# Kernel tuning notes

Measured on AMD Instinct MI355X. Metric: run time of the kernel, lower is better.

The kernel has to match this reference:

```python
import jax, jax.numpy as jnp
import numpy as np

E = 1024   # embed_dim
H = 16     # num_heads
D = E // H # head_dim
B = 2
S = 2048
YAT_EPS = 0.1


def setup_inputs() -> dict:
    key = jax.random.key(0)
    ks = jax.random.split(key, 5)
    w_scale = (6.0 / (E + E)) ** 0.5  # xavier_uniform bound
    def xavier(k):
        return jax.random.uniform(k, (E, E), jnp.float32, -w_scale, w_scale)
    return {
        "x": jax.random.normal(ks[0], (B, S, E), jnp.float32),
        "Wq": xavier(ks[1]), "bq": jnp.zeros((E,), jnp.float32),
        "Wk": xavier(ks[2]), "bk": jnp.zeros((E,), jnp.float32),
        "Wv": xavier(ks[3]), "bv": jnp.zeros((E,), jnp.float32),
        "Wo": xavier(ks[4]), "bo": jnp.zeros((E,), jnp.float32),
    }


def reference(x, Wq, bq, Wk, bk, Wv, bv, Wo, bo):
    b, s, _ = x.shape
    # Projections (Linear: x @ W + b, flax kernel layout [in, out])
    Q = x @ Wq + bq
    K = x @ Wk + bk
    V = x @ Wv + bv
    # [B, H, S, D]
    Q = Q.reshape(b, s, H, D).transpose(0, 2, 1, 3)
    K = K.reshape(b, s, H, D).transpose(0, 2, 1, 3)
    V = V.reshape(b, s, H, D).transpose(0, 2, 1, 3)
    # L2 normalize along head_dim
    Qn = Q / (jnp.linalg.norm(Q, axis=-1, keepdims=True) + 1e-8)
    Kn = K / (jnp.linalg.norm(K, axis=-1, keepdims=True) + 1e-8)
    # Yat kernel scores: (1 + <q,k>)^2 / (eps + (1 - <q,k>))
    dot = jnp.einsum("bhqd,bhkd->bhqk", Qn, Kn)
    scores = (1.0 + dot) ** 2 / (YAT_EPS + (1.0 - dot))
    # Sum-normalize (no softmax)
    attn = scores / (jnp.sum(scores, axis=-1, keepdims=True) + 1e-6)
    out = jnp.einsum("bhqk,bhkd->bhqd", attn, V)
    out = out.transpose(0, 2, 1, 3).reshape(b, s, E)
    return out @ Wo + bo
```

## Files before the change

### kernel.cpp

```cpp
#include <hip/hip_runtime.h>
#include <math.h>

#define EDIM 1024
#define NH   16
#define HD   64
#define BATCH 2
#define SEQ  2048
#define NROW (BATCH*SEQ)
#define YAT_EPS 0.1f

typedef _Float16 f16;
typedef _Float16 f16x8 __attribute__((ext_vector_type(8)));
typedef _Float16 f16x4 __attribute__((ext_vector_type(4)));
typedef __fp16   h16x2 __attribute__((ext_vector_type(2)));
typedef float    f32x4 __attribute__((ext_vector_type(4)));

static __device__ __forceinline__ int pk2(float a, float b) {
    union { h16x2 h; int i; } u;
    u.h = __builtin_amdgcn_cvt_pkrtz(a, b);
    return u.i;
}

static __device__ __forceinline__ void gload16(const f16* g, f16* l) {
    __builtin_amdgcn_global_load_lds(
        (const __attribute__((address_space(1))) void*)g,
        (__attribute__((address_space(3))) void*)l,
        16, 0, 0);
}

__global__ __launch_bounds__(256)
void prep_kernel(const float* __restrict__ x, f16* __restrict__ xb,
                 const float* __restrict__ W0, const float* __restrict__ W1,
                 const float* __restrict__ W2, const float* __restrict__ W3,
                 f16* __restrict__ T0, f16* __restrict__ T1,
                 f16* __restrict__ T2, f16* __restrict__ T3)
{
    const int z = blockIdx.z;
    if (z == 4) {
        const int bid = blockIdx.y * 32 + blockIdx.x;
#pragma unroll
        for (int i = 0; i < 4; ++i) {
            const int off = bid * 4096 + i * 1024 + threadIdx.x * 4;
            const float4 v = *(const float4*)(x + off);
            union { int i2[2]; f16x4 h; } o;
            o.i2[0] = pk2(v.x, v.y);
            o.i2[1] = pk2(v.z, v.w);
            *(f16x4*)(xb + off) = o.h;
        }
        return;
    }
    const float* W = (z == 0) ? W0 : (z == 1) ? W1 : (z == 2) ? W2 : W3;
    f16*         Wt = (z == 0) ? T0 : (z == 1) ? T1 : (z == 2) ? T2 : T3;

    __shared__ float T[32][33];
    const int t = threadIdx.x;
    const int r = t >> 3, c4 = (t & 7) * 4;
    const int bi = blockIdx.x * 32, bj = blockIdx.y * 32;
    const float4 v = *(const float4*)(W + (size_t)(bi + r) * 1024 + bj + c4);
    T[r][c4 + 0] = v.x; T[r][c4 + 1] = v.y; T[r][c4 + 2] = v.z; T[r][c4 + 3] = v.w;
    __syncthreads();
    f16x4 o = {(f16)T[c4 + 0][r], (f16)T[c4 + 1][r], (f16)T[c4 + 2][r], (f16)T[c4 + 3][r]};
    *(f16x4*)(Wt + (size_t)(bj + r) * 1024 + bi + c4) = o;
}

template<int BM, int BN, int WM>
__global__ __launch_bounds__(WM * 128, 3)
void gemm_f16(const f16* __restrict__ A,
              const f16* __restrict__ B0, const f16* __restrict__ B1, const f16* __restrict__ B2,
              const float* __restrict__ bi0, const float* __restrict__ bi1, const float* __restrict__ bi2,
              void* __restrict__ o0, void* __restrict__ o1, void* __restrict__ o2,
              int e0, int e1, int e2)
{
    constexpr int NT    = WM * 128;
    constexpr int SR    = NT / 4;
    constexpr int ASL   = BM / SR;
    constexpr int BSL   = BN / SR;
    constexpr int ABUF  = BM * 32;
    constexpr int BBUF  = BN * 32;
    constexpr int WROWS = BM / WM;
    constexpr int MT    = WROWS / 16;
    constexpr int HALVES = BN / 128;
    constexpr int SCH    = 2048 / NT;
    __shared__ __align__(16) char lds[2 * (ABUF + BBUF) * 2];
    f16* As = (f16*)lds;
    f16* Bs = (f16*)lds + 2 * ABUF;

    const int z = blockIdx.z;
    const f16*   Bt   = (z == 0) ? B0  : (z == 1) ? B1  : B2;
    const float* bias = (z == 0) ? bi0 : (z == 1) ? bi1 : bi2;
    void*        Cout = (z == 0) ? o0  : (z == 1) ? o1  : o2;
    const int    epi  = (z == 0) ? e0  : (z == 1) ? e1  : e2;

    const int tid  = threadIdx.x;
    const int lane = tid & 63;
    const int w    = tid >> 6;
    const int cl   = lane & 15;
    const int quad = lane >> 4;
    const int wm = w % WM, wn = w / WM;
    const int bm = blockIdx.x * BM, bn = blockIdx.y * BN;
    const int wmoff = wm * WROWS;

    const int srow = tid >> 2;
    const int sc   = tid & 3;
    const int scg  = (sc ^ (srow & 3)) * 8;
    const f16* gA = A  + (size_t)(bm + srow) * 1024 + scg;
    const f16* gB = Bt + (size_t)(bn + srow) * 1024 + scg;
    f16* lA[ASL]; f16* lB[BSL];
#pragma unroll
    for (int i = 0; i < ASL; ++i) lA[i] = As + (srow + i * SR) * 32 + sc * 8;
#pragma unroll
    for (int i = 0; i < BSL; ++i) lB[i] = Bs + (srow + i * SR) * 32 + sc * 8;

    f32x4 acc[MT][4];
#pragma unroll
    for (int i = 0; i < MT; ++i)
#pragma unroll
        for (int j = 0; j < 4; ++j) acc[i][j] = (f32x4){0.f, 0.f, 0.f, 0.f};

#pragma unroll
    for (int i = 0; i < ASL; ++i) gload16(gA + (size_t)i * SR * 1024, lA[i]);
#pragma unroll
    for (int i = 0; i < BSL; ++i) gload16(gB + (size_t)i * SR * 1024, lB[i]);
    __syncthreads();

    const int fsw = (quad ^ (cl & 3)) * 8;

    for (int it = 0; it < 32; ++it) {
        const int buf = it & 1, nb = buf ^ 1;
        if (it < 31) {
            const int kn = (it + 1) * 32;
#pragma unroll
            for (int i = 0; i < ASL; ++i)
                gload16(gA + (size_t)i * SR * 1024 + kn, lA[i] + nb * ABUF);
#pragma unroll
            for (int i = 0; i < BSL; ++i)
                gload16(gB + (size_t)i * SR * 1024 + kn, lB[i] + nb * BBUF);
        }
        f16x8 af[MT], bf[4];
#pragma unroll
        for (int mt = 0; mt < MT; ++mt)
            af[mt] = *(const f16x8*)(&As[buf * ABUF + (wmoff + mt * 16 + cl) * 32 + fsw]);
#pragma unroll
        for (int nt = 0; nt < 4; ++nt)
            bf[nt] = *(const f16x8*)(&Bs[buf * BBUF + (wn * 64 + nt * 16 + cl) * 32 + fsw]);
#pragma unroll
        for (int mt = 0; mt < MT; ++mt)
#pragma unroll
            for (int nt = 0; nt < 4; ++nt)
                acc[mt][nt] = __builtin_amdgcn_mfma_f32_16x16x32_f16(af[mt], bf[nt], acc[mt][nt], 0, 0, 0);
        __syncthreads();
    }

    float bcol[4];
#pragma unroll
    for (int nt = 0; nt < 4; ++nt) bcol[nt] = bias[bn + wn * 64 + nt * 16 + cl];
#pragma unroll
    for (int mt = 0; mt < MT; ++mt)
#pragma unroll
        for (int nt = 0; nt < 4; ++nt)
#pragma unroll
            for (int rg = 0; rg < 4; ++rg) acc[mt][nt][rg] += bcol[nt];

    const int b_idx = bm >> 11, sl0 = bm & (SEQ - 1), h0 = bn >> 6;

    if (epi == 0) {
        float* C = (float*)Cout;
#pragma unroll
        for (int mt = 0; mt < MT; ++mt)
#pragma unroll
            for (int rg = 0; rg < 4; ++rg) {
                const int row = bm + wmoff + mt * 16 + quad * 4 + rg;
#pragma unroll
                for (int nt = 0; nt < 4; ++nt)
                    C[(size_t)row * EDIM + bn + wn * 64 + nt * 16 + cl] = acc[mt][nt][rg];
            }
    } else if (epi == 1) {
        if constexpr (BM == 128) {
        f16* C = (f16*)Cout;
        f16* S = (f16*)lds;
#pragma unroll
        for (int h = 0; h < HALVES; ++h) {
            __syncthreads();
            if ((wn >> 1) == h) {
#pragma unroll
                for (int mt = 0; mt < MT; ++mt)
#pragma unroll
                    for (int rg = 0; rg < 4; ++rg) {
                        float ss = 0.f;
#pragma unroll
                        for (int nt = 0; nt < 4; ++nt) ss += acc[mt][nt][rg] * acc[mt][nt][rg];
                        ss += __shfl_xor(ss, 1); ss += __shfl_xor(ss, 2);
                        ss += __shfl_xor(ss, 4); ss += __shfl_xor(ss, 8);
                        const float inv = 1.0f / (sqrtf(ss) + 1e-8f);
                        const int row = wmoff + mt * 16 + quad * 4 + rg;
#pragma unroll
                        for (int nt = 0; nt < 4; ++nt) {
                            const int colh = (wn & 1) * 64 + nt * 16 + cl;
                            S[row * 128 + (((colh >> 3) ^ (row & 15)) * 8) + (colh & 7)] =
                                (f16)(acc[mt][nt][rg] * inv);
                        }
                    }
            }
            __syncthreads();
#pragma unroll
            for (int i = 0; i < SCH; ++i) {
                const int c = tid + i * NT;
                const int s = c >> 4, gi = c & 15;
                f16x8 v = *(const f16x8*)(&S[s * 128 + ((gi ^ (s & 15)) * 8)]);
                const int head = h0 + h * 2 + (gi >> 3), d8 = (gi & 7) * 8;
                *(f16x8*)(C + ((size_t)(b_idx * NH + head) * SEQ + sl0 + s) * HD + d8) = v;
            }
        }
        }
    } else {
        if constexpr (BM == 128) {
        f16* C = (f16*)Cout;
        f16* S = (f16*)lds;
#pragma unroll
        for (int h = 0; h < HALVES; ++h) {
            __syncthreads();
            if ((wn >> 1) == h) {
#pragma unroll
                for (int mt = 0; mt < MT; ++mt) {
                    const int s0 = wmoff + mt * 16 + quad * 4;
#pragma unroll
                    for (int nt = 0; nt < 4; ++nt) {
                        const int colh = (wn & 1) * 64 + nt * 16 + cl;
                        f16x4 o = {(f16)acc[mt][nt][0], (f16)acc[mt][nt][1],
                                   (f16)acc[mt][nt][2], (f16)acc[mt][nt][3]};
                        *(f16x4*)(&S[colh * 128 + (((s0 >> 3) ^ (colh & 15)) * 8) + (s0 & 7)]) = o;
                    }
                }
            }
            __syncthreads();
#pragma unroll
            for (int i = 0; i < SCH; ++i) {
                const int c = tid + i * NT;
                const int colh = c >> 4, gi = c & 15;
                f16x8 v = *(const f16x8*)(&S[colh * 128 + ((gi ^ (colh & 15)) * 8)]);
                const int head = h0 + h * 2 + (colh >> 6), d = colh & 63;
                *(f16x8*)(C + ((size_t)(b_idx * NH + head) * HD + d) * SEQ + sl0 + gi * 8) = v;
            }
        }
        }
    }
}

__global__ __launch_bounds__(512, 4)
void yat_attn(const f16* __restrict__ Qh, const f16* __restrict__ Kh,
              const f16* __restrict__ Vt, f16* __restrict__ AO)
{
    __shared__ __align__(16) char lds[49152];
    f16* Qs = (f16*)lds;
    f16* KB = (f16*)(lds + 16384);
    f16* VB = (f16*)(lds + 32768);

    const int tid  = threadIdx.x;
    const int lane = tid & 63;
    const int w    = tid >> 6;
    const int cl   = lane & 15;
    const int quad = lane >> 4;
    const int wm = w & 3;
    const int wk = w >> 2;
    const int q0 = blockIdx.x * 128;
    const int bh = blockIdx.y;

    const f16* Qg = Qh + (size_t)bh * SEQ * HD;
    const f16* Kg = Kh + (size_t)bh * SEQ * HD;
    const f16* Vg = Vt + (size_t)bh * HD * SEQ;

    const int rkv = tid >> 3;
    const int gkv = tid & 7;
    const f16* gK = Kg + (size_t)rkv * HD + gkv * 8;
    const f16* gV = Vg + (size_t)rkv * SEQ + gkv * 8;
    const int lkOff = rkv * 64 + ((gkv ^ (rkv & 7)) * 8);

    f16x8 kr = *(const f16x8*)(gK);
    f16x8 vr = *(const f16x8*)(gV);

#pragma unroll
    for (int i = 0; i < 2; ++i) {
        const int s0 = tid + i * 512;
        const int row = s0 >> 3, g = s0 & 7;
        f16x8 v = *(const f16x8*)(Qg + (size_t)(q0 + row) * HD + g * 8);
        *(f16x8*)(&Qs[row * 64 + ((g ^ (row & 7)) * 8)]) = v;
    }
    __syncthreads();
    f16x8 qf[2][2];
#pragma unroll
    for (int qt = 0; qt < 2; ++qt)
#pragma unroll
        for (int kb = 0; kb < 2; ++kb)
            qf[qt][kb] = *(const f16x8*)(&Qs[(wm * 32 + qt * 16 + cl) * 64 +
                                             ((kb * 4 + quad) ^ (cl & 7)) * 8]);

    f32x4 O[2][4];
    float rs[2] = {0.f, 0.f};
#pragma unroll
    for (int i = 0; i < 2; ++i)
#pragma unroll
        for (int j = 0; j < 4; ++j) O[i][j] = (f32x4){0.f, 0.f, 0.f, 0.f};

    for (int t = 0; t < 32; ++t) {
        const int buf = t & 1;
        *(f16x8*)(&KB[buf * 4096 + lkOff]) = kr;
        *(f16x8*)(&VB[buf * 4096 + lkOff]) = vr;
        if (t < 31) {
            kr = *(const f16x8*)(gK + (size_t)(t + 1) * 64 * HD);
            vr = *(const f16x8*)(gV + (t + 1) * 64);
        }
        __syncthreads();

        const f16* Ks = KB + buf * 4096;
        const f16* Vs = VB + buf * 4096;

        f32x4 s[2][2];
#pragma unroll
        for (int kt = 0; kt < 2; ++kt)
#pragma unroll
            for (int qt = 0; qt < 2; ++qt) s[kt][qt] = (f32x4){0.f, 0.f, 0.f, 0.f};
#pragma unroll
        for (int kb = 0; kb < 2; ++kb) {
            const int sw = ((kb * 4 + quad) ^ (cl & 7)) * 8;
            f16x8 af0 = *(const f16x8*)(&Ks[(wk * 32 +  0 + cl) * 64 + sw]);
            f16x8 af1 = *(const f16x8*)(&Ks[(wk * 32 + 16 + cl) * 64 + sw]);
#pragma unroll
            for (int qt = 0; qt < 2; ++qt) {
                s[0][qt] = __builtin_amdgcn_mfma_f32_16x16x32_f16(af0, qf[qt][kb], s[0][qt], 0, 0, 0);
                s[1][qt] = __builtin_amdgcn_mfma_f32_16x16x32_f16(af1, qf[qt][kb], s[1][qt], 0, 0, 0);
            }
        }

        f16x4 pa16[2][2];
#pragma unroll
        for (int kt = 0; kt < 2; ++kt)
#pragma unroll
            for (int qt = 0; qt < 2; ++qt) {
                float p[4];
#pragma unroll
                for (int rg = 0; rg < 4; ++rg) {
                    const float u = (1.0f + YAT_EPS) - s[kt][qt][rg];
                    p[rg] = fmaf(4.41f, __builtin_amdgcn_rcpf(u), u - 4.2f);
                    rs[qt] += p[rg];
                }
                union { int i2[2]; f16x4 h; } pk_;
                pk_.i2[0] = pk2(p[0], p[1]);
                pk_.i2[1] = pk2(p[2], p[3]);
                pa16[kt][qt] = pk_.h;
            }

#pragma unroll
        for (int kt = 0; kt < 2; ++kt)
#pragma unroll
            for (int dn = 0; dn < 4; ++dn) {
                const int row = dn * 16 + cl;
                const int g = wk * 4 + kt * 2 + (quad >> 1);
                f16x4 vb = *(const f16x4*)(&Vs[row * 64 + ((g ^ (row & 7)) * 8) + (quad & 1) * 4]);
#pragma unroll
                for (int qt = 0; qt < 2; ++qt)
                    O[qt][dn] = __builtin_amdgcn_mfma_f32_16x16x16f16(pa16[kt][qt], vb, O[qt][dn], 0, 0, 0);
            }
    }

    __syncthreads();
    float* rs_s = (float*)lds;
    float* Ox   = (float*)(lds + 1024);

#pragma unroll
    for (int qt = 0; qt < 2; ++qt) {
        float t = rs[qt];
        t += __shfl_xor(t, 16);
        t += __shfl_xor(t, 32);
        if (quad == 0) rs_s[wk * 128 + wm * 32 + qt * 16 + cl] = t;
    }
    if (wk == 1) {
#pragma unroll
        for (int qt = 0; qt < 2; ++qt)
#pragma unroll
            for (int dn = 0; dn < 4; ++dn)
#pragma unroll
                for (int rg = 0; rg < 4; ++rg)
                    Ox[(wm * 32 + qt * 16 + quad * 4 + rg) * 64 + dn * 16 + cl] = O[qt][dn][rg];
    }
    __syncthreads();
    if (wk == 0) {
        const int b = bh >> 4, h = bh & 15;
#pragma unroll
        for (int qt = 0; qt < 2; ++qt)
#pragma unroll
            for (int rg = 0; rg < 4; ++rg) {
                const int ql = wm * 32 + qt * 16 + quad * 4 + rg;
                const float tot = rs_s[ql] + rs_s[128 + ql];
                const float inv = 1.0f / (tot + 1e-6f);
                const size_t rowoff = ((size_t)b * SEQ + q0 + ql) * EDIM + h * 64;
#pragma unroll
                for (int dn = 0; dn < 4; ++dn)
                    AO[rowoff + dn * 16 + cl] =
                        (f16)((O[qt][dn][rg] + Ox[ql * 64 + dn * 16 + cl]) * inv);
            }
    }
}

extern "C" void kernel_launch(void* const* d_in, const int* in_sizes, int n_in,
                              void* d_out, int out_size, void* d_ws, size_t ws_size,
                              hipStream_t stream)
{
    const float* x  = (const float*)d_in[0];
    const float* Wq = (const float*)d_in[1];
    const float* bq = (const float*)d_in[2];
    const float* Wk = (const float*)d_in[3];
    const float* bk = (const float*)d_in[4];
    const float* Wv = (const float*)d_in[5];
    const float* bv = (const float*)d_in[6];
    const float* Wo = (const float*)d_in[7];
    const float* bo = (const float*)d_in[8];

    char* p = (char*)d_ws;
    f16* xb  = (f16*)p;                 p += (size_t)NROW * EDIM * 2;
    f16* Wqt = (f16*)p;                 p += (size_t)EDIM * EDIM * 2;
    f16* Wkt = (f16*)p;                 p += (size_t)EDIM * EDIM * 2;
    f16* Wvt = (f16*)p;                 p += (size_t)EDIM * EDIM * 2;
    f16* Wot = (f16*)p;                 p += (size_t)EDIM * EDIM * 2;
    f16* Qhb = (f16*)p;                 p += (size_t)NROW * EDIM * 2;
    f16* Khb = (f16*)p;                 p += (size_t)NROW * EDIM * 2;
    f16* Vtb = (f16*)p;                 p += (size_t)NROW * EDIM * 2;
    f16* AOb = (f16*)p;                 p += (size_t)NROW * EDIM * 2;

    prep_kernel<<<dim3(32, 32, 5), 256, 0, stream>>>(x, xb, Wq, Wk, Wv, Wo,
                                                     Wqt, Wkt, Wvt, Wot);

    gemm_f16<128, 128, 4><<<dim3(NROW / 128, EDIM / 128, 3), 512, 0, stream>>>(
        xb, Wqt, Wkt, Wvt, bq, bk, bv, Qhb, Khb, Vtb, 1, 1, 2);

    yat_attn<<<dim3(SEQ / 128, BATCH * NH), 512, 0, stream>>>(Qhb, Khb, Vtb, AOb);

    gemm_f16<64, 128, 2><<<dim3(NROW / 64, EDIM / 128, 1), 256, 0, stream>>>(
        AOb, Wot, Wot, Wot, bo, bo, bo, d_out, d_out, d_out, 0, 0, 0);
}
```

Measured before the change: 197.7 us.

## Split attention over key halves and combine partials in a separate kernel

Splits the attention kernel's key/value loop into two halves along a new grid dimension. Each half writes unnormalized fp32 partial outputs and row sums, and a new combine kernel adds them, normalizes, and writes the f16 attention output. Q fragments are now loaded directly from global memory, which drops the Q LDS staging and shrinks shared memory. Block indices are also remapped to group blocks that share heads. This doubles the block count (512 to 1024) for better occupancy on the many-CU GPU. The cost is extra fp32 partial traffic (about 32MB) and one more kernel launch.

```diff
diff --git a/kernel.cpp b/kernel.cpp
--- a/kernel.cpp
+++ b/kernel.cpp
@@ -248,12 +248,12 @@
 
 __global__ __launch_bounds__(512, 4)
 void yat_attn(const f16* __restrict__ Qh, const f16* __restrict__ Kh,
-              const f16* __restrict__ Vt, f16* __restrict__ AO)
+              const f16* __restrict__ Vt, float* __restrict__ Opart,
+              float* __restrict__ RSpart)
 {
-    __shared__ __align__(16) char lds[49152];
-    f16* Qs = (f16*)lds;
-    f16* KB = (f16*)(lds + 16384);
-    f16* VB = (f16*)(lds + 32768);
+    __shared__ __align__(16) char lds[33792];
+    f16* KB = (f16*)lds;
+    f16* VB = (f16*)(lds + 16384);
 
     const int tid  = threadIdx.x;
     const int lane = tid & 63;
@@ -262,8 +262,12 @@
     const int quad = lane >> 4;
     const int wm = w & 3;
     const int wk = w >> 2;
-    const int q0 = blockIdx.x * 128;
-    const int bh = blockIdx.y;
+    const int ks = blockIdx.z;
+
+    const int old = blockIdx.x + 16 * blockIdx.y;
+    const int nid = (old & 7) * 64 + (old >> 3);
+    const int q0t = nid & 15, bh = nid >> 4;
+    const int q0 = q0t * 128;
 
     const f16* Qg = Qh + (size_t)bh * SEQ * HD;
     const f16* Kg = Kh + (size_t)bh * SEQ * HD;
@@ -271,28 +275,20 @@
 
     const int rkv = tid >> 3;
     const int gkv = tid & 7;
-    const f16* gK = Kg + (size_t)rkv * HD + gkv * 8;
-    const f16* gV = Vg + (size_t)rkv * SEQ + gkv * 8;
+    const f16* gK = Kg + (size_t)(ks * 1024 + rkv) * HD + gkv * 8;
+    const f16* gV = Vg + (size_t)rkv * SEQ + ks * 1024 + gkv * 8;
     const int lkOff = rkv * 64 + ((gkv ^ (rkv & 7)) * 8);
 
     f16x8 kr = *(const f16x8*)(gK);
     f16x8 vr = *(const f16x8*)(gV);
 
-#pragma unroll
-    for (int i = 0; i < 2; ++i) {
-        const int s0 = tid + i * 512;
-        const int row = s0 >> 3, g = s0 & 7;
-        f16x8 v = *(const f16x8*)(Qg + (size_t)(q0 + row) * HD + g * 8);
-        *(f16x8*)(&Qs[row * 64 + ((g ^ (row & 7)) * 8)]) = v;
-    }
-    __syncthreads();
     f16x8 qf[2][2];
 #pragma unroll
     for (int qt = 0; qt < 2; ++qt)
 #pragma unroll
         for (int kb = 0; kb < 2; ++kb)
-            qf[qt][kb] = *(const f16x8*)(&Qs[(wm * 32 + qt * 16 + cl) * 64 +
-                                             ((kb * 4 + quad) ^ (cl & 7)) * 8]);
+            qf[qt][kb] = *(const f16x8*)(Qg + (size_t)(q0 + wm * 32 + qt * 16 + cl) * HD +
+                                         (kb * 4 + quad) * 8);
 
     f32x4 O[2][4];
     float rs[2] = {0.f, 0.f};
@@ -301,11 +297,11 @@
 #pragma unroll
         for (int j = 0; j < 4; ++j) O[i][j] = (f32x4){0.f, 0.f, 0.f, 0.f};
 
-    for (int t = 0; t < 32; ++t) {
+    for (int t = 0; t < 16; ++t) {
         const int buf = t & 1;
         *(f16x8*)(&KB[buf * 4096 + lkOff]) = kr;
         *(f16x8*)(&VB[buf * 4096 + lkOff]) = vr;
-        if (t < 31) {
+        if (t < 15) {
             kr = *(const f16x8*)(gK + (size_t)(t + 1) * 64 * HD);
             vr = *(const f16x8*)(gV + (t + 1) * 64);
         }
@@ -384,20 +380,45 @@
     }
     __syncthreads();
     if (wk == 0) {
-        const int b = bh >> 4, h = bh & 15;
+        float* pO = Opart + ((size_t)(q0t * 32 + bh) * 2 + ks) * 8192;
+        float* pR = RSpart + ((size_t)(q0t * 32 + bh) * 2 + ks) * 128;
 #pragma unroll
         for (int qt = 0; qt < 2; ++qt)
 #pragma unroll
             for (int rg = 0; rg < 4; ++rg) {
                 const int ql = wm * 32 + qt * 16 + quad * 4 + rg;
                 const float tot = rs_s[ql] + rs_s[128 + ql];
-                const float inv = 1.0f / (tot + 1e-6f);
-                const size_t rowoff = ((size_t)b * SEQ + q0 + ql) * EDIM + h * 64;
+                if (cl == 0) pR[ql] = tot;
 #pragma unroll
                 for (int dn = 0; dn < 4; ++dn)
-                    AO[rowoff + dn * 16 + cl] =
-                        (f16)((O[qt][dn][rg] + Ox[ql * 64 + dn * 16 + cl]) * inv);
-            }
+                    pO[ql * 64 + dn * 16 + cl] = O[qt][dn][rg] + Ox[ql * 64 + dn * 16 + cl];
+            }
+    }
+}
+
+__global__ __launch_bounds__(256)
+void attn_combine(const float* __restrict__ Opart, const float* __restrict__ RSpart,
+                  f16* __restrict__ AO)
+{
+    __shared__ float rinv[128];
+    const int bid = blockIdx.x;
+    const int tid = threadIdx.x;
+    const int q0t = bid >> 5, bh = bid & 31, b = bh >> 4, h = bh & 15;
+    const float* O0 = Opart + (size_t)bid * 2 * 8192;
+    const float* O1 = O0 + 8192;
+    const float* R  = RSpart + (size_t)bid * 2 * 128;
+    if (tid < 128) rinv[tid] = 1.0f / (R[tid] + R[128 + tid] + 1e-6f);
+    __syncthreads();
+#pragma unroll
+    for (int c = 0; c < 8; ++c) {
+        const int idx = c * 1024 + tid * 4;
+        const float4 a = *(const float4*)(O0 + idx);
+        const float4 d = *(const float4*)(O1 + idx);
+        const int row = idx >> 6, col = idx & 63;
+        const float inv = rinv[row];
+        f16x4 o = {(f16)((a.x + d.x) * inv), (f16)((a.y + d.y) * inv),
+                   (f16)((a.z + d.z) * inv), (f16)((a.w + d.w) * inv)};
+        *(f16x4*)(AO + ((size_t)b * SEQ + q0t * 128 + row) * EDIM + h * 64 + col) = o;
     }
 }
 
@@ -425,6 +446,8 @@
     f16* Khb = (f16*)p;                 p += (size_t)NROW * EDIM * 2;
     f16* Vtb = (f16*)p;                 p += (size_t)NROW * EDIM * 2;
     f16* AOb = (f16*)p;                 p += (size_t)NROW * EDIM * 2;
+    float* Opart  = (float*)p;          p += (size_t)1024 * 8192 * 4;
+    float* RSpart = (float*)p;          p += (size_t)1024 * 128 * 4;
 
     prep_kernel<<<dim3(32, 32, 5), 256, 0, stream>>>(x, xb, Wq, Wk, Wv, Wo,
                                                      Wqt, Wkt, Wvt, Wot);
@@ -432,7 +455,9 @@
     gemm_f16<128, 128, 4><<<dim3(NROW / 128, EDIM / 128, 3), 512, 0, stream>>>(
         xb, Wqt, Wkt, Wvt, bq, bk, bv, Qhb, Khb, Vtb, 1, 1, 2);
 
-    yat_attn<<<dim3(SEQ / 128, BATCH * NH), 512, 0, stream>>>(Qhb, Khb, Vtb, AOb);
+    yat_attn<<<dim3(SEQ / 128, BATCH * NH, 2), 512, 0, stream>>>(
+        Qhb, Khb, Vtb, Opart, RSpart);
+    attn_combine<<<dim3(512), 256, 0, stream>>>(Opart, RSpart, AOb);
 
     gemm_f16<64, 128, 2><<<dim3(NROW / 64, EDIM / 128, 1), 256, 0, stream>>>(
         AOb, Wot, Wot, Wot, bo, bo, bo, d_out, d_out, d_out, 0, 0, 0);
```

New measurement: 204.0 us. 3.2% more time.

## Software-pipeline QK^T one tile ahead of PV with triple-buffered K/V LDS

Applied to the files above, without the earlier changes.

Restructures the attention loop so the QK^T scores for tile t are computed while the Yat-kernel transform and PV MFMA run on the scores of tile t-1, with a prologue and epilogue. K/V LDS buffers go from double to triple buffering, and Q fragments are loaded straight from global memory instead of staging through LDS. Launch bounds drop from 4 to 2 waves per EU minimum to give room for the extra live score registers. The aim is to overlap MFMA latency with the transcendental math. The cost is higher register pressure and possibly lower occupancy.

```diff
diff --git a/kernel.cpp b/kernel.cpp
--- a/kernel.cpp
+++ b/kernel.cpp
@@ -246,14 +246,13 @@
     }
 }
 
-__global__ __launch_bounds__(512, 4)
+__global__ __launch_bounds__(512, 2)
 void yat_attn(const f16* __restrict__ Qh, const f16* __restrict__ Kh,
               const f16* __restrict__ Vt, f16* __restrict__ AO)
 {
     __shared__ __align__(16) char lds[49152];
-    f16* Qs = (f16*)lds;
-    f16* KB = (f16*)(lds + 16384);
-    f16* VB = (f16*)(lds + 32768);
+    f16* KB = (f16*)lds;
+    f16* VB = (f16*)(lds + 24576);
 
     const int tid  = threadIdx.x;
     const int lane = tid & 63;
@@ -278,21 +277,13 @@
     f16x8 kr = *(const f16x8*)(gK);
     f16x8 vr = *(const f16x8*)(gV);
 
-#pragma unroll
-    for (int i = 0; i < 2; ++i) {
-        const int s0 = tid + i * 512;
-        const int row = s0 >> 3, g = s0 & 7;
-        f16x8 v = *(const f16x8*)(Qg + (size_t)(q0 + row) * HD + g * 8);
-        *(f16x8*)(&Qs[row * 64 + ((g ^ (row & 7)) * 8)]) = v;
-    }
-    __syncthreads();
     f16x8 qf[2][2];
 #pragma unroll
     for (int qt = 0; qt < 2; ++qt)
 #pragma unroll
         for (int kb = 0; kb < 2; ++kb)
-            qf[qt][kb] = *(const f16x8*)(&Qs[(wm * 32 + qt * 16 + cl) * 64 +
-                                             ((kb * 4 + quad) ^ (cl & 7)) * 8]);
+            qf[qt][kb] = *(const f16x8*)(Qg + (size_t)(q0 + wm * 32 + qt * 16 + cl) * HD +
+                                         (kb * 4 + quad) * 8);
 
     f32x4 O[2][4];
     float rs[2] = {0.f, 0.f};
@@ -301,24 +292,48 @@
 #pragma unroll
         for (int j = 0; j < 4; ++j) O[i][j] = (f32x4){0.f, 0.f, 0.f, 0.f};
 
-    for (int t = 0; t < 32; ++t) {
-        const int buf = t & 1;
-        *(f16x8*)(&KB[buf * 4096 + lkOff]) = kr;
-        *(f16x8*)(&VB[buf * 4096 + lkOff]) = vr;
+    *(f16x8*)(&KB[lkOff]) = kr;
+    *(f16x8*)(&VB[lkOff]) = vr;
+    kr = *(const f16x8*)(gK + (size_t)64 * HD);
+    vr = *(const f16x8*)(gV + 64);
+    __syncthreads();
+
+    f32x4 sp[2][2];
+#pragma unroll
+    for (int kt = 0; kt < 2; ++kt)
+#pragma unroll
+        for (int qt = 0; qt < 2; ++qt) sp[kt][qt] = (f32x4){0.f, 0.f, 0.f, 0.f};
+#pragma unroll
+    for (int kb = 0; kb < 2; ++kb) {
+        const int sw = ((kb * 4 + quad) ^ (cl & 7)) * 8;
+        f16x8 af0 = *(const f16x8*)(&KB[(wk * 32 +  0 + cl) * 64 + sw]);
+        f16x8 af1 = *(const f16x8*)(&KB[(wk * 32 + 16 + cl) * 64 + sw]);
+#pragma unroll
+        for (int qt = 0; qt < 2; ++qt) {
+            sp[0][qt] = __builtin_amdgcn_mfma_f32_16x16x32_f16(af0, qf[qt][kb], sp[0][qt], 0, 0, 0);
+            sp[1][qt] = __builtin_amdgcn_mfma_f32_16x16x32_f16(af1, qf[qt][kb], sp[1][qt], 0, 0, 0);
+        }
+    }
+
+    for (int t = 1; t < 32; ++t) {
+        const int wb = t % 3;
+        const int pb = (t - 1) % 3;
+        *(f16x8*)(&KB[wb * 4096 + lkOff]) = kr;
+        *(f16x8*)(&VB[wb * 4096 + lkOff]) = vr;
         if (t < 31) {
             kr = *(const f16x8*)(gK + (size_t)(t + 1) * 64 * HD);
             vr = *(const f16x8*)(gV + (t + 1) * 64);
         }
         __syncthreads();
 
-        const f16* Ks = KB + buf * 4096;
-        const f16* Vs = VB + buf * 4096;
-
-        f32x4 s[2][2];
-#pragma unroll
-        for (int kt = 0; kt < 2; ++kt)
-#pragma unroll
-            for (int qt = 0; qt < 2; ++qt) s[kt][qt] = (f32x4){0.f, 0.f, 0.f, 0.f};
+        const f16* Ks = KB + wb * 4096;
+        const f16* Vs = VB + pb * 4096;
+
+        f32x4 sc[2][2];
+#pragma unroll
+        for (int kt = 0; kt < 2; ++kt)
+#pragma unroll
+            for (int qt = 0; qt < 2; ++qt) sc[kt][qt] = (f32x4){0.f, 0.f, 0.f, 0.f};
 #pragma unroll
         for (int kb = 0; kb < 2; ++kb) {
             const int sw = ((kb * 4 + quad) ^ (cl & 7)) * 8;
@@ -326,8 +341,8 @@
             f16x8 af1 = *(const f16x8*)(&Ks[(wk * 32 + 16 + cl) * 64 + sw]);
 #pragma unroll
             for (int qt = 0; qt < 2; ++qt) {
-                s[0][qt] = __builtin_amdgcn_mfma_f32_16x16x32_f16(af0, qf[qt][kb], s[0][qt], 0, 0, 0);
-                s[1][qt] = __builtin_amdgcn_mfma_f32_16x16x32_f16(af1, qf[qt][kb], s[1][qt], 0, 0, 0);
+                sc[0][qt] = __builtin_amdgcn_mfma_f32_16x16x32_f16(af0, qf[qt][kb], sc[0][qt], 0, 0, 0);
+                sc[1][qt] = __builtin_amdgcn_mfma_f32_16x16x32_f16(af1, qf[qt][kb], sc[1][qt], 0, 0, 0);
             }
         }
 
@@ -339,7 +354,7 @@
                 float p[4];
 #pragma unroll
                 for (int rg = 0; rg < 4; ++rg) {
-                    const float u = (1.0f + YAT_EPS) - s[kt][qt][rg];
+                    const float u = (1.0f + YAT_EPS) - sp[kt][qt][rg];
                     p[rg] = fmaf(4.41f, __builtin_amdgcn_rcpf(u), u - 4.2f);
                     rs[qt] += p[rg];
                 }
@@ -349,6 +364,43 @@
                 pa16[kt][qt] = pk_.h;
             }
 
+#pragma unroll
+        for (int kt = 0; kt < 2; ++kt)
+#pragma unroll
+            for (int dn = 0; dn < 4; ++dn) {
+                const int row = dn * 16 + cl;
+                const int g = wk * 4 + kt * 2 + (quad >> 1);
+                f16x4 vb = *(const f16x4*)(&Vs[row * 64 + ((g ^ (row & 7)) * 8) + (quad & 1) * 4]);
+#pragma unroll
+                for (int qt = 0; qt < 2; ++qt)
+                    O[qt][dn] = __builtin_amdgcn_mfma_f32_16x16x16f16(pa16[kt][qt], vb, O[qt][dn], 0, 0, 0);
+            }
+
+#pragma unroll
+        for (int kt = 0; kt < 2; ++kt)
+#pragma unroll
+            for (int qt = 0; qt < 2; ++qt) sp[kt][qt] = sc[kt][qt];
+    }
+
+    {
+        const f16* Vs = VB + (31 % 3) * 4096;
+        f16x4 pa16[2][2];
+#pragma unroll
+        for (int kt = 0; kt < 2; ++kt)
+#pragma unroll
+            for (int qt = 0; qt < 2; ++qt) {
+                float p[4];
+#pragma unroll
+                for (int rg = 0; rg < 4; ++rg) {
+                    const float u = (1.0f + YAT_EPS) - sp[kt][qt][rg];
+                    p[rg] = fmaf(4.41f, __builtin_amdgcn_rcpf(u), u - 4.2f);
+                    rs[qt] += p[rg];
+                }
+                union { int i2[2]; f16x4 h; } pk_;
+                pk_.i2[0] = pk2(p[0], p[1]);
+                pk_.i2[1] = pk2(p[2], p[3]);
+                pa16[kt][qt] = pk_.h;
+            }
 #pragma unroll
         for (int kt = 0; kt < 2; ++kt)
 #pragma unroll
```

After: 194.5 us. No clear change (-1.6%).
